# Kernel optimization log

Hardware: AMD Instinct MI355X
Metric: run time of the kernel (lower is better)

Reference implementation:

```python
import jax, jax.numpy as jnp
import numpy as np

D_MODEL, D_HEAD, N_HEADS, N_KV_HEADS = 4096, 128, 32, 8
EPS = 1e-5
N = 2048


def rms_norm(x, w, eps):
    return x * jax.lax.rsqrt(jnp.mean(x * x, axis=-1, keepdims=True) + eps) * w


def rope_swap(x):
    # [x0, x1, x2, x3] -> [-x1, x0, -x3, x2]
    xp = x.reshape(x.shape[:-1] + (-1, 2))
    return jnp.stack([-xp[..., 1], xp[..., 0]], axis=-1).reshape(x.shape)


def rope_rotate(x, r_cos, r_sin):
    return x * r_cos + rope_swap(x) * r_sin


def setup_inputs() -> dict:
    key = jax.random.key(0)
    ks = jax.random.split(key, 8)
    sd = 1.0 / np.sqrt(D_MODEL)
    return {
        "x": jax.random.normal(ks[0], (N, D_MODEL), dtype=jnp.float32),
        "r_cos": jax.random.normal(ks[1], (N, D_HEAD), dtype=jnp.float32),
        "r_sin": jax.random.normal(ks[2], (N, D_HEAD), dtype=jnp.float32),
        "w_norm": jnp.ones((D_MODEL,), dtype=jnp.float32),
        "wq": jax.random.normal(ks[3], (D_MODEL, N_HEADS * D_HEAD), dtype=jnp.float32) * sd,
        "wk": jax.random.normal(ks[4], (D_MODEL, N_KV_HEADS * D_HEAD), dtype=jnp.float32) * sd,
        "wv": jax.random.normal(ks[5], (D_MODEL, N_KV_HEADS * D_HEAD), dtype=jnp.float32) * sd,
        "wo": jax.random.normal(ks[6], (D_MODEL, D_MODEL), dtype=jnp.float32) * sd,
    }


def reference(x, r_cos, r_sin, w_norm, wq, wk, wv, wo):
    n = x.shape[0]
    residual = x
    h = rms_norm(x, w_norm, EPS)

    # projections -> [n_heads, n, d_head]
    q = (h @ wq).reshape(n, N_HEADS, D_HEAD).transpose(1, 0, 2)
    k = (h @ wk).reshape(n, N_KV_HEADS, D_HEAD).transpose(1, 0, 2)
    v = (h @ wv).reshape(n, N_KV_HEADS, D_HEAD).transpose(1, 0, 2)

    # GQA: repeat kv heads
    reps = N_HEADS // N_KV_HEADS
    k = jnp.repeat(k, reps, axis=0)
    v = jnp.repeat(v, reps, axis=0)

    q = rope_rotate(q, r_cos, r_sin)
    k = rope_rotate(k, r_cos, r_sin)

    mask = jnp.where(
        jnp.tril(jnp.ones((n, n), dtype=bool)), 0.0, -jnp.inf
    ).astype(x.dtype)
    scores = jnp.einsum("hnd,hmd->hnm", q, k) / np.sqrt(D_HEAD).astype(np.float32) + mask
    a = jnp.einsum("hnm,hmd->hnd", jax.nn.softmax(scores, axis=-1), v)

    a = a.transpose(1, 0, 2).reshape(n, N_HEADS * D_HEAD)
    return residual + a @ wo
```

## Files before the change

### kernel.cpp

```cpp
#include <hip/hip_runtime.h>
#include <stdint.h>
#include <math.h>

#define TOK 2048
#define DMODEL 4096
#define QKV_LD 5120
#define KVB 64
#define PS_LD 72

typedef __attribute__((ext_vector_type(8))) short short8;
typedef __attribute__((ext_vector_type(4))) short short4v;
typedef __attribute__((ext_vector_type(8))) __bf16 bf16x8;
typedef __attribute__((ext_vector_type(4))) float f32x4;

__device__ __forceinline__ unsigned short f2bf(float f) {
  unsigned u = __float_as_uint(f);
  u += 0x7fffu + ((u >> 16) & 1u);
  return (unsigned short)(u >> 16);
}

__device__ __forceinline__ void gl16(const void* g, void* l) {
  __builtin_amdgcn_global_load_lds((__attribute__((address_space(1))) void*)g,
                                   (__attribute__((address_space(3))) void*)l,
                                   16, 0, 0);
}

__device__ __forceinline__ f32x4 mfma16(short8 a, short8 b, f32x4 c) {
  return __builtin_amdgcn_mfma_f32_16x16x32_bf16(__builtin_bit_cast(bf16x8, a),
                                                 __builtin_bit_cast(bf16x8, b),
                                                 c, 0, 0, 0);
}

__device__ __forceinline__ float fexp2(float x) {
  float r;
  asm("v_exp_f32 %0, %1" : "=v"(r) : "v"(x));
  return r;
}

template <int N>
__device__ __forceinline__ void waitvm() {
  if constexpr (N == 0) asm volatile("s_waitcnt vmcnt(0)" ::: "memory");
  else if constexpr (N == 2) asm volatile("s_waitcnt vmcnt(2)" ::: "memory");
  else if constexpr (N == 3) asm volatile("s_waitcnt vmcnt(3)" ::: "memory");
  else static_assert(N == 0 || N == 2 || N == 3, "add literal");
}

__device__ __forceinline__ void waitvm0() {
  asm volatile("s_waitcnt vmcnt(0)" ::: "memory");
}

__global__ __launch_bounds__(256) void k_rmsnorm(const float* __restrict__ x,
                                                 const float* __restrict__ w,
                                                 unsigned short* __restrict__ h) {
  const int row = blockIdx.x;
  const float* xr = x + (size_t)row * DMODEL;
  float4 v[4];
  float ss = 0.f;
#pragma unroll
  for (int i = 0; i < 4; ++i) {
    v[i] = *(const float4*)(xr + threadIdx.x * 4 + i * 1024);
    ss += v[i].x * v[i].x + v[i].y * v[i].y + v[i].z * v[i].z + v[i].w * v[i].w;
  }
#pragma unroll
  for (int m = 1; m < 64; m <<= 1) ss += __shfl_xor(ss, m, 64);
  __shared__ float ws4[4];
  if ((threadIdx.x & 63) == 0) ws4[threadIdx.x >> 6] = ss;
  __syncthreads();
  const float scale = rsqrtf((ws4[0] + ws4[1] + ws4[2] + ws4[3]) * (1.0f / DMODEL) + 1e-5f);
  unsigned short* hr = h + (size_t)row * DMODEL;
#pragma unroll
  for (int i = 0; i < 4; ++i) {
    int col = threadIdx.x * 4 + i * 1024;
    float4 wv = *(const float4*)(w + col);
    uint2 o;
    o.x = (unsigned)f2bf(v[i].x * scale * wv.x) | ((unsigned)f2bf(v[i].y * scale * wv.y) << 16);
    o.y = (unsigned)f2bf(v[i].z * scale * wv.z) | ((unsigned)f2bf(v[i].w * scale * wv.w) << 16);
    *(uint2*)(hr + col) = o;
  }
}

__global__ __launch_bounds__(256) void k_wconvert(const float* __restrict__ W,
                                                  unsigned short* __restrict__ WT,
                                                  int K, int N) {
  __shared__ unsigned short tile[64][65];
  const int n0 = blockIdx.x * 64, k0 = blockIdx.y * 64;
  const int t = threadIdx.x;
  {
    const int r = t >> 2, c0 = (t & 3) * 16;
    const float* src = W + (size_t)(k0 + r) * N + n0 + c0;
#pragma unroll
    for (int i = 0; i < 4; ++i) {
      float4 f = *(const float4*)(src + i * 4);
      tile[r][c0 + i * 4 + 0] = f2bf(f.x);
      tile[r][c0 + i * 4 + 1] = f2bf(f.y);
      tile[r][c0 + i * 4 + 2] = f2bf(f.z);
      tile[r][c0 + i * 4 + 3] = f2bf(f.w);
    }
  }
  __syncthreads();
  {
    const int n = t >> 2, c0 = (t & 3) * 16;
    unsigned short* dst = WT + (size_t)(n0 + n) * K + k0 + c0;
    unsigned short v[16];
#pragma unroll
    for (int i = 0; i < 16; ++i) v[i] = tile[c0 + i][n];
    uint4 o0, o1;
    o0.x = v[0] | ((unsigned)v[1] << 16);  o0.y = v[2] | ((unsigned)v[3] << 16);
    o0.z = v[4] | ((unsigned)v[5] << 16);  o0.w = v[6] | ((unsigned)v[7] << 16);
    o1.x = v[8] | ((unsigned)v[9] << 16);  o1.y = v[10] | ((unsigned)v[11] << 16);
    o1.z = v[12] | ((unsigned)v[13] << 16); o1.w = v[14] | ((unsigned)v[15] << 16);
    *(uint4*)dst = o0;
    *(uint4*)(dst + 8) = o1;
  }
}

__device__ __forceinline__ short8 rdfrag(const unsigned short* buf, int row, int kc) {
  return *(const short8*)((const char*)buf + row * 128 + ((kc ^ (row & 7)) << 4));
}

template <int BM, int BN, int HALF>
__device__ __forceinline__ void stage_half(const unsigned short* __restrict__ A,
                                           const unsigned short* __restrict__ BT,
                                           unsigned short* __restrict__ buf,
                                           int m0, int n0, int K, int kt, int tid) {
  constexpr int LA = BM / 64, LB = BN / 64;
  constexpr int H0A = LA / 2, H0B = (LB + 1) / 2;
  constexpr int A0 = HALF ? H0A : 0, A1 = HALF ? LA : H0A;
  constexpr int B0 = HALF ? H0B : 0, B1 = HALF ? LB : H0B;
  unsigned short* bbuf = buf + BM * 64;
#pragma unroll
  for (int i = A0; i < A1; ++i) {
    const int s = i * 512 + tid, row = s >> 3, ch = s & 7;
    gl16(A + (size_t)(m0 + row) * K + kt + ((ch ^ (row & 7)) << 3), (char*)buf + s * 16);
  }
#pragma unroll
  for (int i = B0; i < B1; ++i) {
    const int s = i * 512 + tid, row = s >> 3, ch = s & 7;
    gl16(BT + (size_t)(n0 + row) * K + kt + ((ch ^ (row & 7)) << 3), (char*)bbuf + s * 16);
  }
}

template <int BM, int BN, int MODE>
__global__ __launch_bounds__(512, 2) void k_gemm_big(const unsigned short* __restrict__ A,
                                                     const unsigned short* __restrict__ BT,
                                                     const float* __restrict__ resid,
                                                     void* __restrict__ Cout,
                                                     unsigned short* __restrict__ vtg,
                                                     const float* __restrict__ rc,
                                                     const float* __restrict__ rs,
                                                     int M, int N, int K) {
  extern __shared__ __align__(16) unsigned short lds[];
  constexpr int MREP = BM / 32;
  constexpr int NREP = BN / 64;
  constexpr int MH = MREP / 2;
  constexpr int TILE = (BM + BN) * 64;
  constexpr int LA = BM / 64, LB = BN / 64;
  constexpr int H0 = LA / 2 + (LB + 1) / 2;

  const int tid = threadIdx.x, lane = tid & 63;
  const int w = tid >> 6, wm = w >> 2, wn = w & 3;
  const int lr = lane & 15, lh = lane >> 4;

  const int wg0 = blockIdx.x;
  const int xcd = wg0 & 7, l = wg0 >> 3;
  const int m0 = (((xcd >> 2) << 3) + (l >> 3)) * BM;
  const int n0 = (((xcd & 3) << 3) + (l & 7)) * BN;

  const f32x4 zf = {0.f, 0.f, 0.f, 0.f};
  f32x4 acc[MREP][NREP];
#pragma unroll
  for (int i = 0; i < MREP; ++i) {
#pragma unroll
    for (int j = 0; j < NREP; ++j) acc[i][j] = zf;
  }

  const int arow0 = wm * (BM / 2);
  const int brow0 = wn * (BN / 4);
  const int NT = K >> 6;
  int cur = 0;

  stage_half<BM, BN, 0>(A, BT, lds, m0, n0, K, 0, tid);
  stage_half<BM, BN, 1>(A, BT, lds, m0, n0, K, 0, tid);

  for (int t = 0; t < NT; ++t) {
    const unsigned short* abuf = lds + cur * TILE;
    const unsigned short* bbuf = abuf + BM * 64;
    unsigned short* nbuf = lds + (cur ^ 1) * TILE;
    const bool pre = (t + 1 < NT);
    const int ktn = (t + 1) << 6;

    short8 bfr[NREP], afr[MH];
    if (pre) {
      stage_half<BM, BN, 0>(A, BT, nbuf, m0, n0, K, ktn, tid);
      waitvm<H0>();
    } else {
      waitvm<0>();
    }
    __builtin_amdgcn_s_barrier();
#pragma unroll
    for (int nr = 0; nr < NREP; ++nr) bfr[nr] = rdfrag(bbuf, brow0 + nr * 16 + lr, lh);
#pragma unroll
    for (int mi = 0; mi < MH; ++mi) afr[mi] = rdfrag(abuf, arow0 + mi * 16 + lr, lh);
    __builtin_amdgcn_s_setprio(1);
#pragma unroll
    for (int mi = 0; mi < MH; ++mi) {
#pragma unroll
      for (int nr = 0; nr < NREP; ++nr)
        acc[mi][nr] = mfma16(afr[mi], bfr[nr], acc[mi][nr]);
    }
    __builtin_amdgcn_s_setprio(0);
    if (pre) stage_half<BM, BN, 1>(A, BT, nbuf, m0, n0, K, ktn, tid);
#pragma unroll
    for (int mi = 0; mi < MH; ++mi) afr[mi] = rdfrag(abuf, arow0 + (MH + mi) * 16 + lr, lh);
    __builtin_amdgcn_s_setprio(1);
#pragma unroll
    for (int mi = 0; mi < MH; ++mi) {
#pragma unroll
      for (int nr = 0; nr < NREP; ++nr)
        acc[MH + mi][nr] = mfma16(afr[mi], bfr[nr], acc[MH + mi][nr]);
    }
    __builtin_amdgcn_s_setprio(0);
#pragma unroll
    for (int nr = 0; nr < NREP; ++nr) bfr[nr] = rdfrag(bbuf, brow0 + nr * 16 + lr, 4 + lh);
#pragma unroll
    for (int mi = 0; mi < MH; ++mi) afr[mi] = rdfrag(abuf, arow0 + mi * 16 + lr, 4 + lh);
    __builtin_amdgcn_s_setprio(1);
#pragma unroll
    for (int mi = 0; mi < MH; ++mi) {
#pragma unroll
      for (int nr = 0; nr < NREP; ++nr)
        acc[mi][nr] = mfma16(afr[mi], bfr[nr], acc[mi][nr]);
    }
    __builtin_amdgcn_s_setprio(0);
#pragma unroll
    for (int mi = 0; mi < MH; ++mi) afr[mi] = rdfrag(abuf, arow0 + (MH + mi) * 16 + lr, 4 + lh);
    asm volatile("s_waitcnt lgkmcnt(0)" ::: "memory");
    __builtin_amdgcn_s_barrier();
    __builtin_amdgcn_s_setprio(1);
#pragma unroll
    for (int mi = 0; mi < MH; ++mi) {
#pragma unroll
      for (int nr = 0; nr < NREP; ++nr)
        acc[MH + mi][nr] = mfma16(afr[mi], bfr[nr], acc[MH + mi][nr]);
    }
    __builtin_amdgcn_s_setprio(0);
    cur ^= 1;
  }

#pragma unroll
  for (int ai = 0; ai < MREP; ++ai) {
#pragma unroll
    for (int ni = 0; ni < NREP; ++ni) {
      const int colg = n0 + wn * (BN / 4) + ni * 16 + lr;
      const int rowg0 = m0 + wm * (BM / 2) + ai * 16 + 4 * lh;
      if (MODE == 1) {
#pragma unroll
        for (int r = 0; r < 4; ++r)
          ((float*)Cout)[(size_t)(rowg0 + r) * N + colg] =
              acc[ai][ni][r] + resid[(size_t)(rowg0 + r) * N + colg];
      } else if (colg >= 5120) {
        short4v o;
#pragma unroll
        for (int r = 0; r < 4; ++r) o[r] = (short)f2bf(acc[ai][ni][r]);
        *(short4v*)(vtg + (size_t)(colg - 5120) * TOK + rowg0) = o;
      } else {
        const int d = colg & 127;
#pragma unroll
        for (int r = 0; r < 4; ++r) {
          const int row = rowg0 + r;
          const float v = acc[ai][ni][r];
          const float p = __shfl_xor(v, 1, 64);
          const float c = rc[row * 128 + d];
          const float s = rs[row * 128 + d];
          const float y = (lr & 1) ? fmaf(p, s, v * c) : fmaf(-p, s, v * c);
          ((unsigned short*)Cout)[(size_t)row * QKV_LD + colg] = f2bf(y);
        }
      }
    }
  }
}

__global__ __launch_bounds__(256) void k_attn(const unsigned short* __restrict__ qkv,
                                              const unsigned short* __restrict__ vtg,
                                              unsigned short* __restrict__ aout) {
  extern __shared__ __align__(16) unsigned short sm[];
  unsigned short* const KsB = sm;
  unsigned short* const VtB = sm + 2 * KVB * 128;
  unsigned short* const Ps = sm + 4 * KVB * 128;
  const int head = blockIdx.y;
  const int hkv = head >> 2;
  const int tid = threadIdx.x, lane = tid & 63, w = tid >> 6;
  const int lr = lane & 15, lh = lane >> 4;
  const float scale2 = 0.08838834764831845f * 1.44269504088896340736f;
  const f32x4 zf = {0.f, 0.f, 0.f, 0.f};

  auto stageKV = [&](int kvt, int buf) {
    unsigned short* Ksn = KsB + buf * (KVB * 128);
    unsigned short* Vtn = VtB + buf * (128 * KVB);
    const int kvn = kvt * KVB;
#pragma unroll
    for (int c = 0; c < 4; ++c) {
      const int s = c * 256 + w * 64 + lane;
      const int row = s >> 4, cp = s & 15;
      gl16(qkv + (size_t)(kvn + row) * QKV_LD + 4096 + hkv * 128 + ((cp ^ (row & 7)) * 8),
           (char*)Ksn + (c * 256 + w * 64) * 16);
    }
#pragma unroll
    for (int c = 0; c < 4; ++c) {
      const int s = c * 256 + w * 64 + lane;
      const int row = s >> 3, cp = s & 7;
      gl16(vtg + (size_t)(hkv * 128 + row) * TOK + kvn + ((cp ^ (row & 7)) * 8),
           (char*)Vtn + (c * 256 + w * 64) * 16);
    }
  };

  for (int half = 0; half < 2; ++half) {
    const int qt = half ? (31 - blockIdx.x) : blockIdx.x;
    const int q0 = qt * 64;

    short8 qf[4];
    {
      const unsigned short* qbase = qkv + (size_t)(q0 + w * 16 + lr) * QKV_LD + head * 128;
#pragma unroll
      for (int kd = 0; kd < 4; ++kd) qf[kd] = *(const short8*)(qbase + kd * 32 + lh * 8);
    }
    f32x4 oacc[8];
#pragma unroll
    for (int vt = 0; vt < 8; ++vt) oacc[vt] = zf;
    float Mr[4], Lp[4];
#pragma unroll
    for (int r = 0; r < 4; ++r) { Mr[r] = -INFINITY; Lp[r] = 0.f; }

    const int nt = qt + 1;
    int cur = 0;
    stageKV(0, 0);

    for (int t = 0; t < nt; ++t) {
      const unsigned short* Ks = KsB + cur * (KVB * 128);
      const unsigned short* Vt = VtB + cur * (128 * KVB);
      const int kv0 = t * KVB;
      waitvm0();
      __builtin_amdgcn_s_barrier();
      __builtin_amdgcn_sched_barrier(0);
      if (t + 1 < nt) stageKV(t + 1, cur ^ 1);

      f32x4 sacc[4];
#pragma unroll
      for (int ct = 0; ct < 4; ++ct) {
        sacc[ct] = zf;
        const int row = ct * 16 + lr;
#pragma unroll
        for (int kd = 0; kd < 4; ++kd) {
          const short8 kf = *(const short8*)((const char*)Ks + row * 256 +
                                             (((kd * 4 + lh) ^ (row & 7)) * 16));
          sacc[ct] = mfma16(qf[kd], kf, sacc[ct]);
        }
      }

      const bool diag = (t == qt);
      float sv[4][4], gmax[4];
#pragma unroll
      for (int r = 0; r < 4; ++r) {
        float s0 = sacc[0][r] * scale2;
        float s1 = sacc[1][r] * scale2;
        float s2 = sacc[2][r] * scale2;
        float s3 = sacc[3][r] * scale2;
        if (diag) {
          const int qrow = q0 + w * 16 + 4 * lh + r;
          if (kv0 + lr > qrow) s0 = -INFINITY;
          if (kv0 + 16 + lr > qrow) s1 = -INFINITY;
          if (kv0 + 32 + lr > qrow) s2 = -INFINITY;
          if (kv0 + 48 + lr > qrow) s3 = -INFINITY;
        }
        float tmax = fmaxf(fmaxf(s0, s1), fmaxf(s2, s3));
        tmax = fmaxf(tmax, __shfl_xor(tmax, 1, 16));
        tmax = fmaxf(tmax, __shfl_xor(tmax, 2, 16));
        tmax = fmaxf(tmax, __shfl_xor(tmax, 4, 16));
        tmax = fmaxf(tmax, __shfl_xor(tmax, 8, 16));
        gmax[r] = tmax;
        sv[r][0] = s0; sv[r][1] = s1; sv[r][2] = s2; sv[r][3] = s3;
      }
      const int cond = (gmax[0] <= Mr[0] + 8.f) && (gmax[1] <= Mr[1] + 8.f) &&
                       (gmax[2] <= Mr[2] + 8.f) && (gmax[3] <= Mr[3] + 8.f);
      if (!__all(cond)) {
        float scv[4];
#pragma unroll
        for (int r = 0; r < 4; ++r) {
          const float mnew = fmaxf(Mr[r], gmax[r]);
          scv[r] = fexp2(Mr[r] - mnew);
          Mr[r] = mnew;
          Lp[r] *= scv[r];
        }
#pragma unroll
        for (int vt = 0; vt < 8; ++vt) {
#pragma unroll
          for (int r = 0; r < 4; ++r) oacc[vt][r] *= scv[r];
        }
      }
      float pv[4][4];
#pragma unroll
      for (int r = 0; r < 4; ++r) {
        const float p0 = fexp2(sv[r][0] - Mr[r]);
        const float p1 = fexp2(sv[r][1] - Mr[r]);
        const float p2 = fexp2(sv[r][2] - Mr[r]);
        const float p3 = fexp2(sv[r][3] - Mr[r]);
        Lp[r] += (p0 + p1) + (p2 + p3);
        pv[r][0] = p0; pv[r][1] = p1; pv[r][2] = p2; pv[r][3] = p3;
      }

      unsigned short* pw = Ps + w * (16 * PS_LD);
#pragma unroll
      for (int r = 0; r < 4; ++r) {
#pragma unroll
        for (int ct = 0; ct < 4; ++ct)
          pw[(4 * lh + r) * PS_LD + ct * 16 + lr] = f2bf(pv[r][ct]);
      }
      asm volatile("s_waitcnt lgkmcnt(0)" ::: "memory");
      short8 pf[2];
      pf[0] = *(const short8*)(pw + lr * PS_LD + lh * 8);
      pf[1] = *(const short8*)(pw + lr * PS_LD + 32 + lh * 8);
      __builtin_amdgcn_s_setprio(1);
#pragma unroll
      for (int vt = 0; vt < 8; ++vt) {
        const int d = vt * 16 + lr;
#pragma unroll
        for (int kb = 0; kb < 2; ++kb) {
          const short8 vf = *(const short8*)((const char*)Vt + d * 128 +
                                             (((kb * 4 + lh) ^ (lr & 7)) * 16));
          oacc[vt] = mfma16(pf[kb], vf, oacc[vt]);
        }
      }
      __builtin_amdgcn_s_setprio(0);
      cur ^= 1;
    }

#pragma unroll
    for (int r = 0; r < 4; ++r) {
      float Ls = Lp[r];
      Ls += __shfl_xor(Ls, 1, 16);
      Ls += __shfl_xor(Ls, 2, 16);
      Ls += __shfl_xor(Ls, 4, 16);
      Ls += __shfl_xor(Ls, 8, 16);
      const float inv = 1.0f / Ls;
      const size_t rowoff = (size_t)(q0 + w * 16 + 4 * lh + r) * DMODEL + head * 128;
#pragma unroll
      for (int vt = 0; vt < 8; ++vt)
        aout[rowoff + vt * 16 + lr] = f2bf(oacc[vt][r] * inv);
    }
    __builtin_amdgcn_s_barrier();
    __builtin_amdgcn_sched_barrier(0);
  }
}

extern "C" void kernel_launch(void* const* d_in, const int* in_sizes, int n_in,
                              void* d_out, int out_size, void* d_ws, size_t ws_size,
                              hipStream_t stream) {
  (void)in_sizes; (void)n_in; (void)out_size; (void)ws_size;
  const float* x     = (const float*)d_in[0];
  const float* r_cos = (const float*)d_in[1];
  const float* r_sin = (const float*)d_in[2];
  const float* wnorm = (const float*)d_in[3];
  const float* wq    = (const float*)d_in[4];
  const float* wk    = (const float*)d_in[5];
  const float* wv    = (const float*)d_in[6];
  const float* wo    = (const float*)d_in[7];

  unsigned short* bufA = (unsigned short*)d_ws;
  unsigned short* qkvb = bufA + (size_t)TOK * DMODEL;
  unsigned short* wT   = qkvb + (size_t)TOK * QKV_LD;
  unsigned short* vtg  = wT + (size_t)6144 * DMODEL;

  hipFuncSetAttribute((const void*)k_gemm_big<128, 192, 0>,
                      hipFuncAttributeMaxDynamicSharedMemorySize, 4 * (128 + 192) * 64);
  hipFuncSetAttribute((const void*)k_gemm_big<128, 128, 1>,
                      hipFuncAttributeMaxDynamicSharedMemorySize, 4 * (128 + 128) * 64);
  const int attn_lds = 4 * KVB * 128 * 2 + 4 * 16 * PS_LD * 2;
  hipFuncSetAttribute((const void*)k_attn,
                      hipFuncAttributeMaxDynamicSharedMemorySize, attn_lds);

  k_rmsnorm<<<TOK, 256, 0, stream>>>(x, wnorm, bufA);
  k_wconvert<<<dim3(64, 64), 256, 0, stream>>>(wq, wT, DMODEL, 4096);
  k_wconvert<<<dim3(16, 64), 256, 0, stream>>>(wk, wT + (size_t)4096 * DMODEL, DMODEL, 1024);
  k_wconvert<<<dim3(16, 64), 256, 0, stream>>>(wv, wT + (size_t)5120 * DMODEL, DMODEL, 1024);
  k_gemm_big<128, 192, 0><<<dim3(512), 512, 4 * (128 + 192) * 64, stream>>>(
      bufA, wT, nullptr, qkvb, vtg, r_cos, r_sin, TOK, 6144, DMODEL);
  k_wconvert<<<dim3(64, 64), 256, 0, stream>>>(wo, wT, DMODEL, 4096);
  k_attn<<<dim3(16, 32), 256, attn_lds, stream>>>(qkvb, vtg, bufA);
  k_gemm_big<128, 128, 1><<<dim3(512), 512, 4 * (128 + 128) * 64, stream>>>(
      bufA, wT, x, d_out, nullptr, nullptr, nullptr, TOK, DMODEL, DMODEL);
}
```

Baseline: 315.0 us.

## Process both causal query tiles concurrently in 512-thread attention blocks sharing KV

The attention kernel now launches 512 threads per block, with two groups of four waves each handling one of the paired query tiles (bx and 31-bx) at the same time. Each KV tile is loaded into LDS once and used by both groups, where before the two tiles were processed one after the other and shared KV tiles were loaded twice. The P staging buffer is changed from a padded stride to an XOR-swizzled layout to avoid LDS bank conflicts. As a trade-off, the short-tile group sits idle through the tail iterations but still joins every barrier, and the larger block may lower occupancy.

```diff
diff --git a/kernel.cpp b/kernel.cpp
--- a/kernel.cpp
+++ b/kernel.cpp
@@ -6,7 +6,6 @@
 #define DMODEL 4096
 #define QKV_LD 5120
 #define KVB 64
-#define PS_LD 72
 
 typedef __attribute__((ext_vector_type(8))) short short8;
 typedef __attribute__((ext_vector_type(4))) short short4v;
@@ -280,7 +279,7 @@
   }
 }
 
-__global__ __launch_bounds__(256) void k_attn(const unsigned short* __restrict__ qkv,
+__global__ __launch_bounds__(512) void k_attn(const unsigned short* __restrict__ qkv,
                                               const unsigned short* __restrict__ vtg,
                                               unsigned short* __restrict__ aout) {
   extern __shared__ __align__(16) unsigned short sm[];
@@ -290,60 +289,63 @@
   const int head = blockIdx.y;
   const int hkv = head >> 2;
   const int tid = threadIdx.x, lane = tid & 63, w = tid >> 6;
+  const int grp = w >> 2, wl = w & 3;
   const int lr = lane & 15, lh = lane >> 4;
   const float scale2 = 0.08838834764831845f * 1.44269504088896340736f;
   const f32x4 zf = {0.f, 0.f, 0.f, 0.f};
+
+  const int bx = blockIdx.x;
+  const int qt = grp ? (31 - bx) : bx;
+  const int q0 = qt * 64;
+  const int ntl = qt + 1;
+  const int NT = 32 - bx;
 
   auto stageKV = [&](int kvt, int buf) {
     unsigned short* Ksn = KsB + buf * (KVB * 128);
     unsigned short* Vtn = VtB + buf * (128 * KVB);
     const int kvn = kvt * KVB;
 #pragma unroll
-    for (int c = 0; c < 4; ++c) {
-      const int s = c * 256 + w * 64 + lane;
+    for (int c = 0; c < 2; ++c) {
+      const int s = c * 512 + tid;
       const int row = s >> 4, cp = s & 15;
       gl16(qkv + (size_t)(kvn + row) * QKV_LD + 4096 + hkv * 128 + ((cp ^ (row & 7)) * 8),
-           (char*)Ksn + (c * 256 + w * 64) * 16);
-    }
-#pragma unroll
-    for (int c = 0; c < 4; ++c) {
-      const int s = c * 256 + w * 64 + lane;
+           (char*)Ksn + (c * 512 + w * 64) * 16);
+    }
+#pragma unroll
+    for (int c = 0; c < 2; ++c) {
+      const int s = c * 512 + tid;
       const int row = s >> 3, cp = s & 7;
       gl16(vtg + (size_t)(hkv * 128 + row) * TOK + kvn + ((cp ^ (row & 7)) * 8),
-           (char*)Vtn + (c * 256 + w * 64) * 16);
+           (char*)Vtn + (c * 512 + w * 64) * 16);
     }
   };
 
-  for (int half = 0; half < 2; ++half) {
-    const int qt = half ? (31 - blockIdx.x) : blockIdx.x;
-    const int q0 = qt * 64;
-
-    short8 qf[4];
-    {
-      const unsigned short* qbase = qkv + (size_t)(q0 + w * 16 + lr) * QKV_LD + head * 128;
-#pragma unroll
-      for (int kd = 0; kd < 4; ++kd) qf[kd] = *(const short8*)(qbase + kd * 32 + lh * 8);
-    }
-    f32x4 oacc[8];
-#pragma unroll
-    for (int vt = 0; vt < 8; ++vt) oacc[vt] = zf;
-    float Mr[4], Lp[4];
-#pragma unroll
-    for (int r = 0; r < 4; ++r) { Mr[r] = -INFINITY; Lp[r] = 0.f; }
-
-    const int nt = qt + 1;
-    int cur = 0;
-    stageKV(0, 0);
-
-    for (int t = 0; t < nt; ++t) {
-      const unsigned short* Ks = KsB + cur * (KVB * 128);
-      const unsigned short* Vt = VtB + cur * (128 * KVB);
-      const int kv0 = t * KVB;
-      waitvm0();
-      __builtin_amdgcn_s_barrier();
-      __builtin_amdgcn_sched_barrier(0);
-      if (t + 1 < nt) stageKV(t + 1, cur ^ 1);
-
+  short8 qf[4];
+  {
+    const unsigned short* qbase = qkv + (size_t)(q0 + wl * 16 + lr) * QKV_LD + head * 128;
+#pragma unroll
+    for (int kd = 0; kd < 4; ++kd) qf[kd] = *(const short8*)(qbase + kd * 32 + lh * 8);
+  }
+  f32x4 oacc[8];
+#pragma unroll
+  for (int vt = 0; vt < 8; ++vt) oacc[vt] = zf;
+  float Mr[4], Lp[4];
+#pragma unroll
+  for (int r = 0; r < 4; ++r) { Mr[r] = -INFINITY; Lp[r] = 0.f; }
+
+  int cur = 0;
+  stageKV(0, 0);
+
+  for (int t = 0; t < NT; ++t) {
+    const unsigned short* Ks = KsB + cur * (KVB * 128);
+    const unsigned short* Vt = VtB + cur * (128 * KVB);
+    const int kv0 = t * KVB;
+    waitvm0();
+    __builtin_amdgcn_s_barrier();
+    __builtin_amdgcn_sched_barrier(0);
+    if (t + 1 < NT) stageKV(t + 1, cur ^ 1);
+
+    if (t < ntl) {
       f32x4 sacc[4];
 #pragma unroll
       for (int ct = 0; ct < 4; ++ct) {
@@ -366,7 +368,7 @@
         float s2 = sacc[2][r] * scale2;
         float s3 = sacc[3][r] * scale2;
         if (diag) {
-          const int qrow = q0 + w * 16 + 4 * lh + r;
+          const int qrow = q0 + wl * 16 + 4 * lh + r;
           if (kv0 + lr > qrow) s0 = -INFINITY;
           if (kv0 + 16 + lr > qrow) s1 = -INFINITY;
           if (kv0 + 32 + lr > qrow) s2 = -INFINITY;
@@ -408,17 +410,19 @@
         pv[r][0] = p0; pv[r][1] = p1; pv[r][2] = p2; pv[r][3] = p3;
       }
 
-      unsigned short* pw = Ps + w * (16 * PS_LD);
+      unsigned short* pw = Ps + w * (16 * 64);
 #pragma unroll
       for (int r = 0; r < 4; ++r) {
+        const int prow = 4 * lh + r;
 #pragma unroll
         for (int ct = 0; ct < 4; ++ct)
-          pw[(4 * lh + r) * PS_LD + ct * 16 + lr] = f2bf(pv[r][ct]);
+          pw[prow * 64 + (((ct * 2 + (lr >> 3)) ^ (prow & 7)) << 3) + (lr & 7)] =
+              f2bf(pv[r][ct]);
       }
       asm volatile("s_waitcnt lgkmcnt(0)" ::: "memory");
       short8 pf[2];
-      pf[0] = *(const short8*)(pw + lr * PS_LD + lh * 8);
-      pf[1] = *(const short8*)(pw + lr * PS_LD + 32 + lh * 8);
+      pf[0] = *(const short8*)((const char*)pw + lr * 128 + (((lh) ^ (lr & 7)) << 4));
+      pf[1] = *(const short8*)((const char*)pw + lr * 128 + (((4 + lh) ^ (lr & 7)) << 4));
       __builtin_amdgcn_s_setprio(1);
 #pragma unroll
       for (int vt = 0; vt < 8; ++vt) {
@@ -431,24 +435,22 @@
         }
       }
       __builtin_amdgcn_s_setprio(0);
-      cur ^= 1;
-    }
-
-#pragma unroll
-    for (int r = 0; r < 4; ++r) {
-      float Ls = Lp[r];
-      Ls += __shfl_xor(Ls, 1, 16);
-      Ls += __shfl_xor(Ls, 2, 16);
-      Ls += __shfl_xor(Ls, 4, 16);
-      Ls += __shfl_xor(Ls, 8, 16);
-      const float inv = 1.0f / Ls;
-      const size_t rowoff = (size_t)(q0 + w * 16 + 4 * lh + r) * DMODEL + head * 128;
-#pragma unroll
-      for (int vt = 0; vt < 8; ++vt)
-        aout[rowoff + vt * 16 + lr] = f2bf(oacc[vt][r] * inv);
-    }
-    __builtin_amdgcn_s_barrier();
-    __builtin_amdgcn_sched_barrier(0);
+    }
+    cur ^= 1;
+  }
+
+#pragma unroll
+  for (int r = 0; r < 4; ++r) {
+    float Ls = Lp[r];
+    Ls += __shfl_xor(Ls, 1, 16);
+    Ls += __shfl_xor(Ls, 2, 16);
+    Ls += __shfl_xor(Ls, 4, 16);
+    Ls += __shfl_xor(Ls, 8, 16);
+    const float inv = 1.0f / Ls;
+    const size_t rowoff = (size_t)(q0 + wl * 16 + 4 * lh + r) * DMODEL + head * 128;
+#pragma unroll
+    for (int vt = 0; vt < 8; ++vt)
+      aout[rowoff + vt * 16 + lr] = f2bf(oacc[vt][r] * inv);
   }
 }
 
@@ -474,7 +476,7 @@
                       hipFuncAttributeMaxDynamicSharedMemorySize, 4 * (128 + 192) * 64);
   hipFuncSetAttribute((const void*)k_gemm_big<128, 128, 1>,
                       hipFuncAttributeMaxDynamicSharedMemorySize, 4 * (128 + 128) * 64);
-  const int attn_lds = 4 * KVB * 128 * 2 + 4 * 16 * PS_LD * 2;
+  const int attn_lds = (4 * KVB * 128 + 8 * 16 * 64) * 2;
   hipFuncSetAttribute((const void*)k_attn,
                       hipFuncAttributeMaxDynamicSharedMemorySize, attn_lds);
 
@@ -485,7 +487,7 @@
   k_gemm_big<128, 192, 0><<<dim3(512), 512, 4 * (128 + 192) * 64, stream>>>(
       bufA, wT, nullptr, qkvb, vtg, r_cos, r_sin, TOK, 6144, DMODEL);
   k_wconvert<<<dim3(64, 64), 256, 0, stream>>>(wo, wT, DMODEL, 4096);
-  k_attn<<<dim3(16, 32), 256, attn_lds, stream>>>(qkvb, vtg, bufA);
+  k_attn<<<dim3(16, 32), 512, attn_lds, stream>>>(qkvb, vtg, bufA);
   k_gemm_big<128, 128, 1><<<dim3(512), 512, 4 * (128 + 128) * 64, stream>>>(
       bufA, wT, x, d_out, nullptr, nullptr, nullptr, TOK, DMODEL, DMODEL);
 }
```

Result: slower. 366.6 us (+16.4%).
